# Performance work log

Measured on AMD Instinct MI355X. Metric: run time of the kernel, lower is better.

## Reference

```python
import jax, jax.numpy as jnp
import numpy as np

NH = 16   # num heads
CS = 16   # inner chunk size

def _gelu(x):
    return jax.nn.gelu(x, approximate=True)

def _diff_gelu(x):
    t = jnp.tanh(0.79788456 * x * (1.0 + 0.044715 * x * x))
    return 0.5 * x * ((1.0 - t * t) * (0.79788456 + 0.1070322243 * x * x)) + 0.5 * (1.0 + t)

def _ln_fused_l2_bwd(x, tgt, gamma, beta, eps=1e-6):
    # x, tgt: [B*nh, CS, f]; gamma/beta: [1, nh, 1, f]
    Bnh, N, HF = x.shape
    mu = x.mean(-1, keepdims=True)
    var = x.var(-1, keepdims=True)
    std = jnp.sqrt(var + eps)
    x_hat = (x - mu) / std
    y = gamma * x_hat.reshape(-1, NH, N, HF) + beta
    go = y - tgt.reshape(-1, NH, N, HF)
    gxh = (go * gamma).reshape(Bnh, N, HF)
    return (HF * gxh - gxh.sum(-1, keepdims=True) - x_hat * (gxh * x_hat).sum(-1, keepdims=True)) / (HF * std)

def setup_inputs() -> dict:
    key = jax.random.key(0)
    ks = jax.random.split(key, 8)
    B, nh, f, hf4, n_chunks = 4, NH, 64, 256, 128
    Bnh = B * nh
    XQ = jax.random.normal(ks[0], (n_chunks, Bnh, CS, f), jnp.float32)
    XK = jax.random.normal(ks[1], (n_chunks, Bnh, CS, f), jnp.float32)
    XV = jax.random.normal(ks[2], (n_chunks, Bnh, CS, f), jnp.float32)
    # inner-loop lr coeffs (ilr * token_idx ~ lr/head_dim): small positive
    coeff = jax.random.uniform(ks[3], (n_chunks, Bnh, CS, 1), jnp.float32) * 0.01
    coeff_last = jax.random.uniform(ks[4], (n_chunks, Bnh, 1, 1), jnp.float32) * 0.01
    W1 = jax.random.normal(ks[5], (Bnh, f, hf4), jnp.float32) * 0.02
    b1 = jnp.zeros((Bnh, 1, hf4), jnp.float32)
    W2 = jax.random.normal(ks[6], (Bnh, hf4, f), jnp.float32) * 0.02
    b2 = jnp.zeros((Bnh, 1, f), jnp.float32)
    ln_weight = jnp.ones((1, nh, 1, f), jnp.float32)
    ln_bias = jnp.zeros((1, nh, 1, f), jnp.float32)
    return dict(XQ=XQ, XK=XK, XV=XV, coeff=coeff, coeff_last=coeff_last,
                W1=W1, b1=b1, W2=W2, b2=b2, ln_weight=ln_weight, ln_bias=ln_bias)

def reference(XQ, XK, XV, coeff, coeff_last, W1, b1, W2, b2, ln_weight, ln_bias):
    n_chunks, Bnh, _, f = XQ.shape
    attn_b = jnp.tril(jnp.ones((CS, CS), XQ.dtype))

    def step(carry, inp):
        W1c, b1c, W2c, b2c = carry
        xv, xk, xq, c, cl = inp
        Z1 = xk @ W1c + b1c                      # [Bnh, CS, 4f]
        X2 = _gelu(Z1)
        Z2 = X2 @ W2c + b2c                      # [Bnh, CS, f]
        dZ2 = _ln_fused_l2_bwd(Z2, xv - xk, ln_weight, ln_bias)
        dZ1 = (dZ2 @ W2c.transpose(0, 2, 1)) * _diff_gelu(Z1)
        b1_bar = b1c - c * (attn_b @ dZ1)
        A1 = jnp.tril(xq @ xk.transpose(0, 2, 1))
        Z1_bar = xq @ W1c - c * (A1 @ dZ1) + b1_bar
        X2_bar = _gelu(Z1_bar)
        b2_bar = b2c - c * (attn_b @ dZ2)
        A2 = jnp.tril(X2_bar @ X2.transpose(0, 2, 1))
        Z2_bar = X2_bar @ W2c - c * (A2 @ dZ2) + b2_bar
        W1n = W1c - cl * (xk.transpose(0, 2, 1) @ dZ1)
        W2n = W2c - cl * (X2.transpose(0, 2, 1) @ dZ2)
        return (W1n, b1_bar[:, -1:], W2n, b2_bar[:, -1:]), Z2_bar

    _, Z2_all = jax.lax.scan(step, (W1, b1, W2, b2), (XV, XK, XQ, coeff, coeff_last))
    # [n_chunks, Bnh, CS, f] -> [Bnh, N, f]
    return Z2_all.transpose(1, 0, 2, 3).reshape(Bnh, n_chunks * CS, f)
```

## Files before the change

### kernel.cpp

```cpp
#include <hip/hip_runtime.h>

typedef __attribute__((ext_vector_type(8))) short bf16x8;
typedef __attribute__((ext_vector_type(4))) float f32x4;

#define MFMA16(a,b,c) __builtin_amdgcn_mfma_f32_16x16x32_bf16(a,b,c,0,0,0)
#define A_GELU 0.7978845608028654f

#define OFF_W1B   0u
#define OFF_W2F   36864u
#define OFF_XK    70656u
#define OFF_XQ    72960u
#define OFF_X2    75264u
#define OFF_X2B   83712u
#define OFF_DZ2B  92160u
#define OFF_DZ1CT 94464u
#define OFF_DZ2CT 114944u
#define OFF_M1    120064u
#define OFF_M2    121344u
#define OFF_Z2F   122624u
#define OFF_TGT   126976u
#define OFF_B2    131072u
#define OFF_COEF  131584u
#define OFF_CL    131648u
#define SMEM_BYTES 131712u

__device__ __forceinline__ float fast_tanh(float u){
    float e = __expf(2.0f*u);
    return 1.0f - 2.0f/(e + 1.0f);
}
__device__ __forceinline__ float gelu_f(float x){
    float t = fast_tanh(A_GELU*(x + 0.044715f*x*x*x));
    return 0.5f*x*(1.0f+t);
}
__device__ __forceinline__ float dgelu_f(float x){
    float x2 = x*x;
    float t = fast_tanh(A_GELU*x*(1.0f + 0.044715f*x2));
    return 0.5f*x*((1.0f-t*t)*(A_GELU + 0.1070322243f*x2)) + 0.5f*(1.0f+t);
}
__device__ __forceinline__ short f2bf(float f){
    unsigned u = __builtin_bit_cast(unsigned, f);
    u += 0x7FFFu + ((u >> 16) & 1u);
    return (short)(u >> 16);
}
__device__ __forceinline__ float bf2f(unsigned short s){
    unsigned u = ((unsigned)s) << 16;
    return __builtin_bit_cast(float, u);
}
__device__ __forceinline__ bf16x8 ldfrag(const unsigned short* p){
    return *(const bf16x8*)p;
}

__global__ __launch_bounds__(512, 1)
void ttt_m2(const float* __restrict__ XQ, const float* __restrict__ XK,
            const float* __restrict__ XV, const float* __restrict__ coeff,
            const float* __restrict__ coeff_last,
            const float* __restrict__ W1g, const float* __restrict__ b1g,
            const float* __restrict__ W2g, const float* __restrict__ b2g,
            const float* __restrict__ gammag, const float* __restrict__ betag,
            float* __restrict__ out)
{
    const int h  = blockIdx.x;
    const int t  = threadIdx.x;
    const int l  = t & 63;
    const int w  = t >> 6;
    const int lo = l & 15;
    const int hi = l >> 4;

    extern __shared__ char smem[];
    unsigned short* sW1bu  = (unsigned short*)(smem + OFF_W1B);
    unsigned short* sW2fu  = (unsigned short*)(smem + OFF_W2F);
    unsigned short* sxku   = (unsigned short*)(smem + OFF_XK);
    unsigned short* sxqu   = (unsigned short*)(smem + OFF_XQ);
    unsigned short* sX2u   = (unsigned short*)(smem + OFF_X2);
    unsigned short* sX2bu  = (unsigned short*)(smem + OFF_X2B);
    unsigned short* sdZ2bu = (unsigned short*)(smem + OFF_DZ2B);
    unsigned short* sdZ1ct = (unsigned short*)(smem + OFF_DZ1CT);
    unsigned short* sdZ2ct = (unsigned short*)(smem + OFF_DZ2CT);
    unsigned short* sM1u   = (unsigned short*)(smem + OFF_M1);
    unsigned short* sM2u   = (unsigned short*)(smem + OFF_M2);
    float* sZ2f  = (float*)(smem + OFF_Z2F);
    float* stgt  = (float*)(smem + OFF_TGT);
    float* b2f   = (float*)(smem + OFF_B2);
    float* scoef = (float*)(smem + OFF_COEF);
    float* sCL   = (float*)(smem + OFF_CL);

    const int base1 = h*16384;
    const int base2 = h*16384;

    float mW1[4][2][4];
    float mW2[2][4][4];
    #pragma unroll
    for (int mt = 0; mt < 4; ++mt)
      #pragma unroll
      for (int tix = 0; tix < 2; ++tix)
        #pragma unroll
        for (int reg = 0; reg < 4; ++reg) {
            const int m = mt*16 + hi*4 + reg, n = (2*w + tix)*16 + lo;
            mW1[mt][tix][reg] = W1g[base1 + m*256 + n];
        }
    #pragma unroll
    for (int mi = 0; mi < 2; ++mi)
      #pragma unroll
      for (int nt = 0; nt < 4; ++nt)
        #pragma unroll
        for (int reg = 0; reg < 4; ++reg) {
            const int m = (2*w + mi)*16 + hi*4 + reg, n = nt*16 + lo;
            mW2[mi][nt][reg] = W2g[base2 + m*64 + n];
        }
    float b1reg[2];
    b1reg[0] = b1g[h*256 + (2*w)*16 + lo];
    b1reg[1] = b1g[h*256 + (2*w+1)*16 + lo];

    for (int i = 0; i < 32; ++i) {
        const int idx = i*512 + t;
        const int m = idx >> 8, n = idx & 255;
        sW1bu[n*72 + m] = f2bf(W1g[base1 + idx]);
    }
    for (int i = 0; i < 32; ++i) {
        const int idx = i*512 + t;
        const int hf = idx >> 6, f = idx & 63;
        sW2fu[f*264 + hf] = f2bf(W2g[base2 + idx]);
    }
    if (t < 64) b2f[t] = b2g[h*64 + t];
    if (t < 256) {
        for (int k = 16; k < 40; ++k) sdZ1ct[t*40 + k] = 0;
    }
    if (t < 64) {
        for (int k = 16; k < 40; ++k) sdZ2ct[t*40 + k] = 0;
    }
    if (t < 16) {
        for (int k = 16; k < 40; ++k) { sM1u[t*40 + k] = 0; sM2u[t*40 + k] = 0; }
    }

    const float gj = gammag[(h & 15)*64 + l];
    const float bj = betag [(h & 15)*64 + l];
    __syncthreads();

    for (int ci = 0; ci < 128; ++ci) {
        const int cb = ci*65536 + h*1024;

        #pragma unroll
        for (int i = 0; i < 2; ++i) {
            const int r = w*2 + i;
            const float xkv = XK[cb + r*64 + l];
            const float xqv = XQ[cb + r*64 + l];
            const float xvv = XV[cb + r*64 + l];
            sxku[r*72 + l] = f2bf(xkv);
            sxqu[r*72 + l] = f2bf(xqv);
            stgt[r*64 + l] = xvv - xkv;
        }
        if (t < 16)  scoef[t] = coeff[ci*1024 + h*16 + t];
        if (t == 16) sCL[0]   = coeff_last[ci*64 + h];
        __syncthreads();
        const float clv = sCL[0];
        const float c15 = scoef[15];

        float z1s[8];
        bf16x8 afk0 = ldfrag(sxku + lo*72 + hi*8);
        bf16x8 afk1 = ldfrag(sxku + lo*72 + 32 + hi*8);
        #pragma unroll
        for (int tix = 0; tix < 2; ++tix) {
            const int n = (2*w + tix)*16 + lo;
            f32x4 acc = {b1reg[tix], b1reg[tix], b1reg[tix], b1reg[tix]};
            acc = MFMA16(afk0, ldfrag(sW1bu + n*72 + hi*8), acc);
            acc = MFMA16(afk1, ldfrag(sW1bu + n*72 + 32 + hi*8), acc);
            #pragma unroll
            for (int reg = 0; reg < 4; ++reg) {
                z1s[tix*4 + reg] = acc[reg];
                sX2u[(hi*4 + reg)*264 + n] = f2bf(gelu_f(acc[reg]));
            }
        }
        if (w == 0) {
            bf16x8 aq0 = ldfrag(sxqu + lo*72 + hi*8);
            bf16x8 aq1 = ldfrag(sxqu + lo*72 + 32 + hi*8);
            f32x4 a1 = {0.f, 0.f, 0.f, 0.f};
            a1 = MFMA16(aq0, afk0, a1);
            a1 = MFMA16(aq1, afk1, a1);
            #pragma unroll
            for (int reg = 0; reg < 4; ++reg) {
                const int r = hi*4 + reg;
                const float cr = scoef[r];
                const float v = (lo <= r) ? (-cr*(a1[reg] + 1.0f)) : 0.0f;
                sM1u[r*40 + lo] = f2bf(v);
            }
        }
        __syncthreads();

        const int tile = w & 3, kh = w >> 2;
        const int nf = tile*16 + lo;
        f32x4 accPB;
        if (kh == 0) {
            const float b2v = b2f[(ci & 1)*64 + nf];
            accPB = (f32x4){b2v, b2v, b2v, b2v};
        } else accPB = (f32x4){0.f, 0.f, 0.f, 0.f};
        #pragma unroll
        for (int s = 0; s < 4; ++s) {
            const int k = (kh*4 + s)*32 + hi*8;
            accPB = MFMA16(ldfrag(sX2u + lo*264 + k),
                           ldfrag(sW2fu + nf*264 + k), accPB);
        }
        if (kh == 1) {
            #pragma unroll
            for (int reg = 0; reg < 4; ++reg)
                sZ2f[(hi*4 + reg)*68 + nf] = accPB[reg];
        }
        __syncthreads();
        if (kh == 0) {
            #pragma unroll
            for (int reg = 0; reg < 4; ++reg)
                sZ2f[(hi*4 + reg)*68 + nf] += accPB[reg];
        }
        __syncthreads();

        #pragma unroll
        for (int i = 0; i < 2; ++i) {
            const int r = w*2 + i;
            const float z2 = sZ2f[r*68 + l];
            float s1 = z2, s2 = z2*z2;
            #pragma unroll
            for (int m = 1; m < 64; m <<= 1) { s1 += __shfl_xor(s1, m); s2 += __shfl_xor(s2, m); }
            const float mu   = s1*(1.0f/64.0f);
            const float var  = s2*(1.0f/64.0f) - mu*mu;
            const float rstd = rsqrtf(var + 1e-6f);
            const float xh   = (z2 - mu)*rstd;
            const float go   = gj*xh + bj - stgt[r*64 + l];
            const float gg   = go*gj;
            float u1 = gg, u2 = gg*xh;
            #pragma unroll
            for (int m = 1; m < 64; m <<= 1) { u1 += __shfl_xor(u1, m); u2 += __shfl_xor(u2, m); }
            const float dz2 = (64.0f*gg - u1 - xh*u2)*(rstd*(1.0f/64.0f));
            const short hv = f2bf(dz2);
            sdZ2bu[r*72 + l]  = hv;
            sdZ2ct[l*40 + r]  = hv;
        }
        __syncthreads();

        float b1old[2];
        {
            bf16x8 ad0 = ldfrag(sdZ2bu + lo*72 + hi*8);
            bf16x8 ad1 = ldfrag(sdZ2bu + lo*72 + 32 + hi*8);
            #pragma unroll
            for (int tix = 0; tix < 2; ++tix) {
                const int n = (2*w + tix)*16 + lo;
                f32x4 acc = {0.f, 0.f, 0.f, 0.f};
                bf16x8 bw;
                #pragma unroll
                for (int j = 0; j < 8; ++j) bw[j] = (short)sW2fu[(hi*8 + j)*264 + n];
                acc = MFMA16(ad0, bw, acc);
                #pragma unroll
                for (int j = 0; j < 8; ++j) bw[j] = (short)sW2fu[(32 + hi*8 + j)*264 + n];
                acc = MFMA16(ad1, bw, acc);
                float cs = 0.f;
                #pragma unroll
                for (int reg = 0; reg < 4; ++reg) {
                    const int r = hi*4 + reg;
                    const float dz1v = acc[reg]*dgelu_f(z1s[tix*4 + reg]);
                    sdZ1ct[n*40 + r] = f2bf(dz1v);
                    cs += dz1v;
                }
                cs += __shfl_xor(cs, 16);
                cs += __shfl_xor(cs, 32);
                b1old[tix] = b1reg[tix];
                b1reg[tix] -= c15*cs;
            }
        }
        __syncthreads();

        {
            bf16x8 aq0 = ldfrag(sxqu + lo*72 + hi*8);
            bf16x8 aq1 = ldfrag(sxqu + lo*72 + 32 + hi*8);
            bf16x8 am1 = ldfrag(sM1u + lo*40 + hi*8);
            #pragma unroll
            for (int tix = 0; tix < 2; ++tix) {
                const int n = (2*w + tix)*16 + lo;
                f32x4 acc = {b1old[tix], b1old[tix], b1old[tix], b1old[tix]};
                acc = MFMA16(aq0, ldfrag(sW1bu + n*72 + hi*8), acc);
                acc = MFMA16(aq1, ldfrag(sW1bu + n*72 + 32 + hi*8), acc);
                acc = MFMA16(am1, ldfrag(sdZ1ct + n*40 + hi*8), acc);
                #pragma unroll
                for (int reg = 0; reg < 4; ++reg)
                    sX2bu[(hi*4 + reg)*264 + n] = f2bf(gelu_f(acc[reg]));
            }
            bf16x8 bz0 = ldfrag(sdZ1ct + ((2*w)*16 + lo)*40 + hi*8);
            bf16x8 bz1 = ldfrag(sdZ1ct + ((2*w+1)*16 + lo)*40 + hi*8);
            #pragma unroll
            for (int mt = 0; mt < 4; ++mt) {
                bf16x8 axt = (bf16x8){0,0,0,0,0,0,0,0};
                if (l < 32) {
                    #pragma unroll
                    for (int j = 0; j < 8; ++j)
                        axt[j] = (short)sxku[(hi*8 + j)*72 + (mt*16 + lo)];
                }
                f32x4 z4 = {0.f,0.f,0.f,0.f};
                f32x4 u0 = MFMA16(axt, bz0, z4);
                f32x4 u1 = MFMA16(axt, bz1, z4);
                #pragma unroll
                for (int reg = 0; reg < 4; ++reg) {
                    mW1[mt][0][reg] -= clv*u0[reg];
                    mW1[mt][1][reg] -= clv*u1[reg];
                }
            }
        }
        __syncthreads();

        {
            bf16x8 bz2[4];
            #pragma unroll
            for (int nt = 0; nt < 4; ++nt)
                bz2[nt] = ldfrag(sdZ2ct + (nt*16 + lo)*40 + hi*8);
            #pragma unroll
            for (int mi = 0; mi < 2; ++mi) {
                const int mt = 2*w + mi;
                bf16x8 ax2 = (bf16x8){0,0,0,0,0,0,0,0};
                if (l < 32) {
                    #pragma unroll
                    for (int j = 0; j < 8; ++j)
                        ax2[j] = (short)sX2u[(hi*8 + j)*264 + (mt*16 + lo)];
                }
                #pragma unroll
                for (int nt = 0; nt < 4; ++nt) {
                    f32x4 z4 = {0.f,0.f,0.f,0.f};
                    f32x4 u = MFMA16(ax2, bz2[nt], z4);
                    #pragma unroll
                    for (int reg = 0; reg < 4; ++reg)
                        mW2[mi][nt][reg] -= clv*u[reg];
                }
            }
            if (w == 0) {
                f32x4 a2 = {0.f,0.f,0.f,0.f};
                #pragma unroll
                for (int ks = 0; ks < 8; ++ks) {
                    const int k = ks*32 + hi*8;
                    a2 = MFMA16(ldfrag(sX2bu + lo*264 + k),
                                ldfrag(sX2u + lo*264 + k), a2);
                }
                #pragma unroll
                for (int reg = 0; reg < 4; ++reg) {
                    const int r = hi*4 + reg;
                    const float cr = scoef[r];
                    const float v = (lo <= r) ? (-cr*(a2[reg] + 1.0f)) : 0.0f;
                    sM2u[r*40 + lo] = f2bf(v);
                }
            }
            if (w == 1) {
                float cs = 0.f;
                #pragma unroll
                for (int k = 0; k < 16; ++k) cs += bf2f(sdZ2ct[l*40 + k]);
                b2f[((ci+1) & 1)*64 + l] = b2f[(ci & 1)*64 + l] - c15*cs;
            }
        }
        __syncthreads();

        f32x4 accPF;
        if (kh == 0) {
            const float b2v = b2f[(ci & 1)*64 + nf];
            accPF = (f32x4){b2v, b2v, b2v, b2v};
        } else accPF = (f32x4){0.f, 0.f, 0.f, 0.f};
        #pragma unroll
        for (int s = 0; s < 4; ++s) {
            const int k = (kh*4 + s)*32 + hi*8;
            accPF = MFMA16(ldfrag(sX2bu + lo*264 + k),
                           ldfrag(sW2fu + nf*264 + k), accPF);
        }
        if (kh == 0) {
            accPF = MFMA16(ldfrag(sM2u + lo*40 + hi*8),
                           ldfrag(sdZ2ct + nf*40 + hi*8), accPF);
        } else {
            #pragma unroll
            for (int reg = 0; reg < 4; ++reg)
                sZ2f[(hi*4 + reg)*68 + nf] = accPF[reg];
        }
        __syncthreads();

        if (kh == 0) {
            #pragma unroll
            for (int reg = 0; reg < 4; ++reg) {
                const int r = hi*4 + reg;
                out[h*131072 + (ci*16 + r)*64 + nf] = accPF[reg] + sZ2f[r*68 + nf];
            }
        }
        #pragma unroll
        for (int mt = 0; mt < 4; ++mt)
          #pragma unroll
          for (int tix = 0; tix < 2; ++tix)
            #pragma unroll
            for (int reg = 0; reg < 4; ++reg) {
                const int m = mt*16 + hi*4 + reg, n = (2*w + tix)*16 + lo;
                sW1bu[n*72 + m] = f2bf(mW1[mt][tix][reg]);
            }
        #pragma unroll
        for (int mi = 0; mi < 2; ++mi)
          #pragma unroll
          for (int nt = 0; nt < 4; ++nt)
            #pragma unroll
            for (int reg = 0; reg < 4; ++reg) {
                const int m = (2*w + mi)*16 + hi*4 + reg, n = nt*16 + lo;
                sW2fu[n*264 + m] = f2bf(mW2[mi][nt][reg]);
            }
        __syncthreads();
    }
}

extern "C" void kernel_launch(void* const* d_in, const int* in_sizes, int n_in,
                              void* d_out, int out_size, void* d_ws, size_t ws_size,
                              hipStream_t stream) {
    const float* XQ  = (const float*)d_in[0];
    const float* XK  = (const float*)d_in[1];
    const float* XV  = (const float*)d_in[2];
    const float* cf  = (const float*)d_in[3];
    const float* cfl = (const float*)d_in[4];
    const float* W1  = (const float*)d_in[5];
    const float* b1  = (const float*)d_in[6];
    const float* W2  = (const float*)d_in[7];
    const float* b2  = (const float*)d_in[8];
    const float* gam = (const float*)d_in[9];
    const float* bet = (const float*)d_in[10];
    float* o = (float*)d_out;

    hipFuncSetAttribute((const void*)ttt_m2,
                        hipFuncAttributeMaxDynamicSharedMemorySize, SMEM_BYTES);
    ttt_m2<<<64, 512, SMEM_BYTES, stream>>>(XQ, XK, XV, cf, cfl, W1, b1, W2, b2, gam, bet, o);
}
```

Before: 1.041 ms.

## Add transposed LDS copies, XOR-swizzle W2, pack bf16 conversions, drop a barrier

Adds transposed LDS buffers for XK and X2 so the weight-update MFMAs load their A fragments as vectors instead of gathering them element by element. It also XOR-swizzles the W2 LDS layout to cut bank conflicts on the strided transposed reads. All bf16 conversions now use the packed v_cvt_pk_bf16_f32 instruction with wider stores. The two split-K Z2 partial sums go to separate buffers, which removes one barrier. In exchange, LDS use grows to about 161KB and some extra stores are needed per chunk.

Result: slower. 1.070 ms (+2.8%).

```diff
diff --git a/kernel.cpp b/kernel.cpp
--- a/kernel.cpp
+++ b/kernel.cpp
@@ -2,6 +2,7 @@
 
 typedef __attribute__((ext_vector_type(8))) short bf16x8;
 typedef __attribute__((ext_vector_type(4))) float f32x4;
+typedef __attribute__((ext_vector_type(2))) unsigned int u32x2;
 
 #define MFMA16(a,b,c) __builtin_amdgcn_mfma_f32_16x16x32_bf16(a,b,c,0,0,0)
 #define A_GELU 0.7978845608028654f
@@ -15,14 +16,19 @@
 #define OFF_DZ2B  92160u
 #define OFF_DZ1CT 94464u
 #define OFF_DZ2CT 114944u
-#define OFF_M1    120064u
-#define OFF_M2    121344u
-#define OFF_Z2F   122624u
-#define OFF_TGT   126976u
-#define OFF_B2    131072u
-#define OFF_COEF  131584u
-#define OFF_CL    131648u
-#define SMEM_BYTES 131712u
+#define OFF_XKCT  120064u
+#define OFF_X2CT  125184u
+#define OFF_M1    145664u
+#define OFF_M2    146944u
+#define OFF_Z2F   148224u
+#define OFF_Z2G   152576u
+#define OFF_TGT   156928u
+#define OFF_B2    161024u
+#define OFF_COEF  161536u
+#define OFF_CL    161600u
+#define SMEM_BYTES 161616u
+
+#define W2COL(col, row) ((col) ^ (((row)&7)<<3))
 
 __device__ __forceinline__ float fast_tanh(float u){
     float e = __expf(2.0f*u);
@@ -45,6 +51,11 @@
 __device__ __forceinline__ float bf2f(unsigned short s){
     unsigned u = ((unsigned)s) << 16;
     return __builtin_bit_cast(float, u);
+}
+__device__ __forceinline__ unsigned pkbf(float a, float b){
+    unsigned r;
+    asm("v_cvt_pk_bf16_f32 %0, %1, %2" : "=v"(r) : "v"(a), "v"(b));
+    return r;
 }
 __device__ __forceinline__ bf16x8 ldfrag(const unsigned short* p){
     return *(const bf16x8*)p;
@@ -76,9 +87,12 @@
     unsigned short* sdZ2bu = (unsigned short*)(smem + OFF_DZ2B);
     unsigned short* sdZ1ct = (unsigned short*)(smem + OFF_DZ1CT);
     unsigned short* sdZ2ct = (unsigned short*)(smem + OFF_DZ2CT);
+    unsigned short* sxkct  = (unsigned short*)(smem + OFF_XKCT);
+    unsigned short* sX2ct  = (unsigned short*)(smem + OFF_X2CT);
     unsigned short* sM1u   = (unsigned short*)(smem + OFF_M1);
     unsigned short* sM2u   = (unsigned short*)(smem + OFF_M2);
     float* sZ2f  = (float*)(smem + OFF_Z2F);
+    float* sZ2g  = (float*)(smem + OFF_Z2G);
     float* stgt  = (float*)(smem + OFF_TGT);
     float* b2f   = (float*)(smem + OFF_B2);
     float* scoef = (float*)(smem + OFF_COEF);
@@ -119,14 +133,14 @@
     for (int i = 0; i < 32; ++i) {
         const int idx = i*512 + t;
         const int hf = idx >> 6, f = idx & 63;
-        sW2fu[f*264 + hf] = f2bf(W2g[base2 + idx]);
+        sW2fu[f*264 + W2COL(hf, f)] = f2bf(W2g[base2 + idx]);
     }
     if (t < 64) b2f[t] = b2g[h*64 + t];
     if (t < 256) {
-        for (int k = 16; k < 40; ++k) sdZ1ct[t*40 + k] = 0;
+        for (int k = 16; k < 40; ++k) { sdZ1ct[t*40 + k] = 0; sX2ct[t*40 + k] = 0; }
     }
     if (t < 64) {
-        for (int k = 16; k < 40; ++k) sdZ2ct[t*40 + k] = 0;
+        for (int k = 16; k < 40; ++k) { sdZ2ct[t*40 + k] = 0; sxkct[t*40 + k] = 0; }
     }
     if (t < 16) {
         for (int k = 16; k < 40; ++k) { sM1u[t*40 + k] = 0; sM2u[t*40 + k] = 0; }
@@ -139,15 +153,20 @@
     for (int ci = 0; ci < 128; ++ci) {
         const int cb = ci*65536 + h*1024;
 
-        #pragma unroll
-        for (int i = 0; i < 2; ++i) {
-            const int r = w*2 + i;
-            const float xkv = XK[cb + r*64 + l];
-            const float xqv = XQ[cb + r*64 + l];
-            const float xvv = XV[cb + r*64 + l];
-            sxku[r*72 + l] = f2bf(xkv);
-            sxqu[r*72 + l] = f2bf(xqv);
-            stgt[r*64 + l] = xvv - xkv;
+        {
+            const int r0 = w*2;
+            const float xk0 = XK[cb + r0*64 + l],     xq0 = XQ[cb + r0*64 + l];
+            const float xk1 = XK[cb + (r0+1)*64 + l], xq1 = XQ[cb + (r0+1)*64 + l];
+            const float xv0 = XV[cb + r0*64 + l],     xv1 = XV[cb + (r0+1)*64 + l];
+            const unsigned pkk = pkbf(xk0, xk1);
+            const unsigned pkq = pkbf(xq0, xq1);
+            sxku[r0*72 + l]     = (unsigned short)pkk;
+            sxku[(r0+1)*72 + l] = (unsigned short)(pkk >> 16);
+            sxqu[r0*72 + l]     = (unsigned short)pkq;
+            sxqu[(r0+1)*72 + l] = (unsigned short)(pkq >> 16);
+            *(unsigned*)&sxkct[l*40 + r0] = pkk;
+            stgt[r0*64 + l]     = xv0 - xk0;
+            stgt[(r0+1)*64 + l] = xv1 - xk1;
         }
         if (t < 16)  scoef[t] = coeff[ci*1024 + h*16 + t];
         if (t == 16) sCL[0]   = coeff_last[ci*64 + h];
@@ -164,11 +183,18 @@
             f32x4 acc = {b1reg[tix], b1reg[tix], b1reg[tix], b1reg[tix]};
             acc = MFMA16(afk0, ldfrag(sW1bu + n*72 + hi*8), acc);
             acc = MFMA16(afk1, ldfrag(sW1bu + n*72 + 32 + hi*8), acc);
+            float g[4];
             #pragma unroll
             for (int reg = 0; reg < 4; ++reg) {
                 z1s[tix*4 + reg] = acc[reg];
-                sX2u[(hi*4 + reg)*264 + n] = f2bf(gelu_f(acc[reg]));
-            }
+                g[reg] = gelu_f(acc[reg]);
+            }
+            const unsigned p01 = pkbf(g[0], g[1]), p23 = pkbf(g[2], g[3]);
+            sX2u[(hi*4+0)*264 + n] = (unsigned short)p01;
+            sX2u[(hi*4+1)*264 + n] = (unsigned short)(p01 >> 16);
+            sX2u[(hi*4+2)*264 + n] = (unsigned short)p23;
+            sX2u[(hi*4+3)*264 + n] = (unsigned short)(p23 >> 16);
+            *(u32x2*)&sX2ct[n*40 + hi*4] = (u32x2){p01, p23};
         }
         if (w == 0) {
             bf16x8 aq0 = ldfrag(sxqu + lo*72 + hi*8);
@@ -188,50 +214,49 @@
 
         const int tile = w & 3, kh = w >> 2;
         const int nf = tile*16 + lo;
-        f32x4 accPB;
-        if (kh == 0) {
-            const float b2v = b2f[(ci & 1)*64 + nf];
-            accPB = (f32x4){b2v, b2v, b2v, b2v};
-        } else accPB = (f32x4){0.f, 0.f, 0.f, 0.f};
-        #pragma unroll
-        for (int s = 0; s < 4; ++s) {
-            const int k = (kh*4 + s)*32 + hi*8;
-            accPB = MFMA16(ldfrag(sX2u + lo*264 + k),
-                           ldfrag(sW2fu + nf*264 + k), accPB);
-        }
-        if (kh == 1) {
+        {
+            f32x4 accPB;
+            if (kh == 0) {
+                const float b2v = b2f[(ci & 1)*64 + nf];
+                accPB = (f32x4){b2v, b2v, b2v, b2v};
+            } else accPB = (f32x4){0.f, 0.f, 0.f, 0.f};
+            #pragma unroll
+            for (int s = 0; s < 4; ++s) {
+                const int k = (kh*4 + s)*32 + hi*8;
+                accPB = MFMA16(ldfrag(sX2u + lo*264 + k),
+                               ldfrag(sW2fu + nf*264 + W2COL(k, nf)), accPB);
+            }
+            float* dst = (kh == 0) ? sZ2g : sZ2f;
             #pragma unroll
             for (int reg = 0; reg < 4; ++reg)
-                sZ2f[(hi*4 + reg)*68 + nf] = accPB[reg];
-        }
-        __syncthreads();
-        if (kh == 0) {
-            #pragma unroll
-            for (int reg = 0; reg < 4; ++reg)
-                sZ2f[(hi*4 + reg)*68 + nf] += accPB[reg];
-        }
-        __syncthreads();
-
-        #pragma unroll
-        for (int i = 0; i < 2; ++i) {
-            const int r = w*2 + i;
-            const float z2 = sZ2f[r*68 + l];
-            float s1 = z2, s2 = z2*z2;
-            #pragma unroll
-            for (int m = 1; m < 64; m <<= 1) { s1 += __shfl_xor(s1, m); s2 += __shfl_xor(s2, m); }
-            const float mu   = s1*(1.0f/64.0f);
-            const float var  = s2*(1.0f/64.0f) - mu*mu;
-            const float rstd = rsqrtf(var + 1e-6f);
-            const float xh   = (z2 - mu)*rstd;
-            const float go   = gj*xh + bj - stgt[r*64 + l];
-            const float gg   = go*gj;
-            float u1 = gg, u2 = gg*xh;
-            #pragma unroll
-            for (int m = 1; m < 64; m <<= 1) { u1 += __shfl_xor(u1, m); u2 += __shfl_xor(u2, m); }
-            const float dz2 = (64.0f*gg - u1 - xh*u2)*(rstd*(1.0f/64.0f));
-            const short hv = f2bf(dz2);
-            sdZ2bu[r*72 + l]  = hv;
-            sdZ2ct[l*40 + r]  = hv;
+                dst[(hi*4 + reg)*68 + nf] = accPB[reg];
+        }
+        __syncthreads();
+
+        {
+            float dzp[2];
+            #pragma unroll
+            for (int i = 0; i < 2; ++i) {
+                const int r = w*2 + i;
+                const float z2 = sZ2f[r*68 + l] + sZ2g[r*68 + l];
+                float s1 = z2, s2 = z2*z2;
+                #pragma unroll
+                for (int m = 1; m < 64; m <<= 1) { s1 += __shfl_xor(s1, m); s2 += __shfl_xor(s2, m); }
+                const float mu   = s1*(1.0f/64.0f);
+                const float var  = s2*(1.0f/64.0f) - mu*mu;
+                const float rstd = rsqrtf(var + 1e-6f);
+                const float xh   = (z2 - mu)*rstd;
+                const float go   = gj*xh + bj - stgt[r*64 + l];
+                const float gg   = go*gj;
+                float u1 = gg, u2 = gg*xh;
+                #pragma unroll
+                for (int m = 1; m < 64; m <<= 1) { u1 += __shfl_xor(u1, m); u2 += __shfl_xor(u2, m); }
+                dzp[i] = (64.0f*gg - u1 - xh*u2)*(rstd*(1.0f/64.0f));
+            }
+            const unsigned pk = pkbf(dzp[0], dzp[1]);
+            sdZ2bu[(w*2)*72 + l]   = (unsigned short)pk;
+            sdZ2bu[(w*2+1)*72 + l] = (unsigned short)(pk >> 16);
+            *(unsigned*)&sdZ2ct[l*40 + w*2] = pk;
         }
         __syncthreads();
 
@@ -245,19 +270,22 @@
                 f32x4 acc = {0.f, 0.f, 0.f, 0.f};
                 bf16x8 bw;
                 #pragma unroll
-                for (int j = 0; j < 8; ++j) bw[j] = (short)sW2fu[(hi*8 + j)*264 + n];
+                for (int j = 0; j < 8; ++j)
+                    bw[j] = (short)sW2fu[(hi*8 + j)*264 + (n ^ (j<<3))];
                 acc = MFMA16(ad0, bw, acc);
                 #pragma unroll
-                for (int j = 0; j < 8; ++j) bw[j] = (short)sW2fu[(32 + hi*8 + j)*264 + n];
+                for (int j = 0; j < 8; ++j)
+                    bw[j] = (short)sW2fu[(32 + hi*8 + j)*264 + (n ^ (j<<3))];
                 acc = MFMA16(ad1, bw, acc);
+                float dv[4];
                 float cs = 0.f;
                 #pragma unroll
                 for (int reg = 0; reg < 4; ++reg) {
-                    const int r = hi*4 + reg;
-                    const float dz1v = acc[reg]*dgelu_f(z1s[tix*4 + reg]);
-                    sdZ1ct[n*40 + r] = f2bf(dz1v);
-                    cs += dz1v;
+                    dv[reg] = acc[reg]*dgelu_f(z1s[tix*4 + reg]);
+                    cs += dv[reg];
                 }
+                *(u32x2*)&sdZ1ct[n*40 + hi*4] =
+                    (u32x2){pkbf(dv[0], dv[1]), pkbf(dv[2], dv[3])};
                 cs += __shfl_xor(cs, 16);
                 cs += __shfl_xor(cs, 32);
                 b1old[tix] = b1reg[tix];
@@ -277,20 +305,20 @@
                 acc = MFMA16(aq0, ldfrag(sW1bu + n*72 + hi*8), acc);
                 acc = MFMA16(aq1, ldfrag(sW1bu + n*72 + 32 + hi*8), acc);
                 acc = MFMA16(am1, ldfrag(sdZ1ct + n*40 + hi*8), acc);
-                #pragma unroll
-                for (int reg = 0; reg < 4; ++reg)
-                    sX2bu[(hi*4 + reg)*264 + n] = f2bf(gelu_f(acc[reg]));
+                float g[4];
+                #pragma unroll
+                for (int reg = 0; reg < 4; ++reg) g[reg] = gelu_f(acc[reg]);
+                const unsigned p01 = pkbf(g[0], g[1]), p23 = pkbf(g[2], g[3]);
+                sX2bu[(hi*4+0)*264 + n] = (unsigned short)p01;
+                sX2bu[(hi*4+1)*264 + n] = (unsigned short)(p01 >> 16);
+                sX2bu[(hi*4+2)*264 + n] = (unsigned short)p23;
+                sX2bu[(hi*4+3)*264 + n] = (unsigned short)(p23 >> 16);
             }
             bf16x8 bz0 = ldfrag(sdZ1ct + ((2*w)*16 + lo)*40 + hi*8);
             bf16x8 bz1 = ldfrag(sdZ1ct + ((2*w+1)*16 + lo)*40 + hi*8);
             #pragma unroll
             for (int mt = 0; mt < 4; ++mt) {
-                bf16x8 axt = (bf16x8){0,0,0,0,0,0,0,0};
-                if (l < 32) {
-                    #pragma unroll
-                    for (int j = 0; j < 8; ++j)
-                        axt[j] = (short)sxku[(hi*8 + j)*72 + (mt*16 + lo)];
-                }
+                bf16x8 axt = ldfrag(sxkct + (mt*16 + lo)*40 + hi*8);
                 f32x4 z4 = {0.f,0.f,0.f,0.f};
                 f32x4 u0 = MFMA16(axt, bz0, z4);
                 f32x4 u1 = MFMA16(axt, bz1, z4);
@@ -310,13 +338,7 @@
                 bz2[nt] = ldfrag(sdZ2ct + (nt*16 + lo)*40 + hi*8);
             #pragma unroll
             for (int mi = 0; mi < 2; ++mi) {
-                const int mt = 2*w + mi;
-                bf16x8 ax2 = (bf16x8){0,0,0,0,0,0,0,0};
-                if (l < 32) {
-                    #pragma unroll
-                    for (int j = 0; j < 8; ++j)
-                        ax2[j] = (short)sX2u[(hi*8 + j)*264 + (mt*16 + lo)];
-                }
+                bf16x8 ax2 = ldfrag(sX2ct + ((2*w + mi)*16 + lo)*40 + hi*8);
                 #pragma unroll
                 for (int nt = 0; nt < 4; ++nt) {
                     f32x4 z4 = {0.f,0.f,0.f,0.f};
@@ -360,7 +382,7 @@
         for (int s = 0; s < 4; ++s) {
             const int k = (kh*4 + s)*32 + hi*8;
             accPF = MFMA16(ldfrag(sX2bu + lo*264 + k),
-                           ldfrag(sW2fu + nf*264 + k), accPF);
+                           ldfrag(sW2fu + nf*264 + W2COL(k, nf)), accPF);
         }
         if (kh == 0) {
             accPF = MFMA16(ldfrag(sM2u + lo*40 + hi*8),
@@ -382,21 +404,21 @@
         #pragma unroll
         for (int mt = 0; mt < 4; ++mt)
           #pragma unroll
-          for (int tix = 0; tix < 2; ++tix)
-            #pragma unroll
-            for (int reg = 0; reg < 4; ++reg) {
-                const int m = mt*16 + hi*4 + reg, n = (2*w + tix)*16 + lo;
-                sW1bu[n*72 + m] = f2bf(mW1[mt][tix][reg]);
-            }
+          for (int tix = 0; tix < 2; ++tix) {
+                const int n = (2*w + tix)*16 + lo, m0 = mt*16 + hi*4;
+                *(u32x2*)&sW1bu[n*72 + m0] =
+                    (u32x2){pkbf(mW1[mt][tix][0], mW1[mt][tix][1]),
+                            pkbf(mW1[mt][tix][2], mW1[mt][tix][3])};
+          }
         #pragma unroll
         for (int mi = 0; mi < 2; ++mi)
           #pragma unroll
-          for (int nt = 0; nt < 4; ++nt)
-            #pragma unroll
-            for (int reg = 0; reg < 4; ++reg) {
-                const int m = (2*w + mi)*16 + hi*4 + reg, n = nt*16 + lo;
-                sW2fu[n*264 + m] = f2bf(mW2[mi][nt][reg]);
-            }
+          for (int nt = 0; nt < 4; ++nt) {
+                const int n = nt*16 + lo, m0 = (2*w + mi)*16 + hi*4;
+                *(u32x2*)&sW2fu[n*264 + (m0 ^ ((n&7)<<3))] =
+                    (u32x2){pkbf(mW2[mi][nt][0], mW2[mi][nt][1]),
+                            pkbf(mW2[mi][nt][2], mW2[mi][nt][3])};
+          }
         __syncthreads();
     }
 }
```
